# Optimization experiments

Hardware: AMD Instinct MI355X
Metric: run time of the kernel (lower is better)

Reference implementation:

```python
import jax, jax.numpy as jnp
import numpy as np

N_NODES = 50000
N_EDGES = 800000
IN_FEAT = 256
HEADS = 8
D_K = 64


def setup_inputs() -> dict:
    key = jax.random.key(0)
    ks = jax.random.split(key, 6)
    x = jax.random.normal(ks[0], (N_NODES, IN_FEAT), dtype=jnp.float32)
    edge_index = jax.random.randint(ks[1], (2, N_EDGES), 0, N_NODES, dtype=jnp.int32)
    # xavier-uniform linear weights, stored as [in, out] for x @ W
    limit = float(np.sqrt(6.0 / (IN_FEAT + HEADS * D_K)))
    Wq = jax.random.uniform(ks[2], (IN_FEAT, HEADS * D_K), jnp.float32, -limit, limit)
    Wk = jax.random.uniform(ks[3], (IN_FEAT, HEADS * D_K), jnp.float32, -limit, limit)
    Wv = jax.random.uniform(ks[4], (IN_FEAT, HEADS * D_K), jnp.float32, -limit, limit)
    D = jax.random.uniform(ks[5], (HEADS, D_K), jnp.float32, -1.0, 1.0)
    return {"x": x, "edge_index": edge_index, "Wq": Wq, "Wk": Wk, "Wv": Wv, "D": D}


def reference(x, edge_index, Wq, Wk, Wv, D):
    N = x.shape[0]
    H, dk = D.shape
    scale = 1.0 / np.sqrt(dk)

    Q = (x @ Wq).reshape(N, H, dk)
    K = (x @ Wk).reshape(N, H, dk)
    V = (x @ Wv).reshape(N, H, dk)

    row, col = edge_index[0], edge_index[1]
    Ke = K[row]          # [E, H, dk]
    Qe = Q[col]          # [E, H, dk] (for self edges col==row so Q[col]==Q[row])
    diff = Ke - Qe
    s_edge = jnp.einsum('ehd,hd->eh', diff * diff, D)   # diagonal Mahalanobis
    s_self = jnp.einsum('ehd,hd->eh', Ke * Qe, D)       # self-loop score
    scores = jnp.where((row == col)[:, None], s_self, s_edge)
    scores = jax.nn.leaky_relu(scores * scale, negative_slope=0.2)

    # segment softmax over destination node `row` (PyG softmax semantics)
    smax = jax.ops.segment_max(scores, row, num_segments=N)
    smax = jnp.where(jnp.isfinite(smax), smax, 0.0)     # nodes with no incoming edges
    ex = jnp.exp(scores - smax[row])
    denom = jax.ops.segment_sum(ex, row, num_segments=N)
    alpha = ex / (denom[row] + 1e-16)                   # [E, H]

    out = jax.ops.segment_sum(alpha[:, :, None] * V[col], row, num_segments=N)
    return out.reshape(N, H * dk)
```

## Files before the change

kernel.cpp:

```cpp
#include <hip/hip_runtime.h>
#include <hip/hip_bf16.h>

#define N_NODES 50000
#define N_PAD   50176
#define N_EDGES 800000
#define IN_FEAT 256
#define HEADS 8
#define D_K 64
#define HD 512

typedef __hip_bfloat16 bf16;
typedef unsigned int u32;

using bf16x8 = __attribute__((ext_vector_type(8))) short;
using f32x4  = __attribute__((ext_vector_type(4))) float;

#define WS_Q       0
#define WS_K       51200000
#define WS_V       102400000
#define WS_OFFSETS 153600000
#define WS_CURSOR  153800192
#define WS_DEG     154000192
#define WS_CSR     154200192
#define WS_SQ2     157400192
#define WS_AUX     159000192

#define DOUT_XB 0
#define DOUT_WT 25690112

#define SCAN_BLOCKS 49

__device__ __forceinline__ float bflo(u32 u) { return __uint_as_float(u << 16); }
__device__ __forceinline__ float bfhi(u32 u) { return __uint_as_float(u & 0xffff0000u); }

__device__ __forceinline__ void gload16(const void* g, void* l)
{
    __builtin_amdgcn_global_load_lds(
        (const __attribute__((address_space(1))) unsigned int*)g,
        (__attribute__((address_space(3))) unsigned int*)l,
        16, 0, 0);
}

__global__ __launch_bounds__(256) void convert_x(
    const float* __restrict__ x, bf16* __restrict__ xb)
{
    const int t   = blockIdx.x * 256 + threadIdx.x;
    const int row = t >> 5;
    const int c8  = (t & 31) * 8;
    if (row >= N_PAD) return;
    alignas(16) bf16 tmp[8];
    if (row < N_NODES) {
        const float* p = x + (size_t)row * IN_FEAT + c8;
        float4 a = *(const float4*)p;
        float4 b = *(const float4*)(p + 4);
        tmp[0] = __float2bfloat16(a.x); tmp[1] = __float2bfloat16(a.y);
        tmp[2] = __float2bfloat16(a.z); tmp[3] = __float2bfloat16(a.w);
        tmp[4] = __float2bfloat16(b.x); tmp[5] = __float2bfloat16(b.y);
        tmp[6] = __float2bfloat16(b.z); tmp[7] = __float2bfloat16(b.w);
    } else {
#pragma unroll
        for (int i = 0; i < 8; ++i) tmp[i] = __float2bfloat16(0.f);
    }
    *(uint4*)(xb + (size_t)row * IN_FEAT + c8) = *(const uint4*)tmp;
}

__global__ __launch_bounds__(256) void convert_w(
    const float* __restrict__ Wq, const float* __restrict__ Wk, const float* __restrict__ Wv,
    bf16* __restrict__ Wt)
{
    const int t = blockIdx.x * 256 + threadIdx.x;
    if (t >= 3 * 512 * 256) return;
    const int mat = t >> 17;
    const int r   = t & 131071;
    const int n   = r >> 8;
    const int k   = r & 255;
    const float* W = (mat == 0) ? Wq : (mat == 1) ? Wk : Wv;
    Wt[t] = __float2bfloat16(W[k * HD + n]);
}

__global__ __launch_bounds__(256) void mfma_qkv(
    const bf16* __restrict__ xb, const bf16* __restrict__ Wt,
    bf16* __restrict__ Qb, bf16* __restrict__ Kb, bf16* __restrict__ Vb)
{
    __shared__ uint4 Ab4[512];
    __shared__ uint4 Bb4[512];
    char* AbB = (char*)Ab4;
    char* BbB = (char*)Bb4;

    const int tid  = threadIdx.x;
    const int lane = tid & 63;
    const int wid  = tid >> 6;
    const int wr   = wid >> 1;
    const int wc   = wid & 1;

    const int m0  = blockIdx.x * 128;
    const int n0  = blockIdx.y * 128;
    const int mat = blockIdx.z;
    const bf16* __restrict__ wt = Wt + (size_t)mat * 512 * 256;
    bf16* __restrict__ outp = (mat == 0) ? Qb : (mat == 1) ? Kb : Vb;

    const int rch  = lane >> 2;
    const int slot = (lane & 3) ^ (rch & 3);
    const int sc0  = wid;
    const int sc1  = wid + 4;
    const size_t arow0 = (size_t)(m0 + sc0 * 16 + rch) * IN_FEAT + slot * 8;
    const size_t arow1 = (size_t)(m0 + sc1 * 16 + rch) * IN_FEAT + slot * 8;
    const size_t brow0 = (size_t)(n0 + sc0 * 16 + rch) * IN_FEAT + slot * 8;
    const size_t brow1 = (size_t)(n0 + sc1 * 16 + rch) * IN_FEAT + slot * 8;

    const int fr    = lane & 15;
    const int fslot = (((lane >> 4) ^ (lane & 3)) << 4);
    const int abase = (wr * 64 + fr) * 64 + fslot;
    const int bbase = (wc * 64 + fr) * 64 + fslot;

    f32x4 acc[4][4];
#pragma unroll
    for (int i = 0; i < 4; ++i)
#pragma unroll
        for (int j = 0; j < 4; ++j) acc[i][j] = {0.f, 0.f, 0.f, 0.f};

    for (int k0 = 0; k0 < IN_FEAT; k0 += 32) {
        gload16(xb + arow0 + k0, AbB + sc0 * 1024);
        gload16(xb + arow1 + k0, AbB + sc1 * 1024);
        gload16(wt + brow0 + k0, BbB + sc0 * 1024);
        gload16(wt + brow1 + k0, BbB + sc1 * 1024);
        __syncthreads();

        bf16x8 aF[4], bF[4];
#pragma unroll
        for (int m = 0; m < 4; ++m) aF[m] = *(const bf16x8*)(AbB + abase + m * 16 * 64);
#pragma unroll
        for (int n = 0; n < 4; ++n) bF[n] = *(const bf16x8*)(BbB + bbase + n * 16 * 64);
#pragma unroll
        for (int m = 0; m < 4; ++m)
#pragma unroll
            for (int n = 0; n < 4; ++n)
                acc[m][n] = __builtin_amdgcn_mfma_f32_16x16x32_bf16(aF[m], bF[n], acc[m][n], 0, 0, 0);
        __syncthreads();
    }

    const int c_col = lane & 15;
    const int r_hi  = (lane >> 4) * 4;
#pragma unroll
    for (int m = 0; m < 4; ++m) {
        const int grow_base = m0 + wr * 64 + m * 16 + r_hi;
#pragma unroll
        for (int j = 0; j < 4; ++j) {
            const int grow = grow_base + j;
            if (grow < N_NODES) {
#pragma unroll
                for (int n = 0; n < 4; ++n)
                    outp[(size_t)grow * HD + n0 + wc * 64 + n * 16 + c_col] =
                        __float2bfloat16(acc[m][n][j]);
            }
        }
    }
}

__global__ void zero_deg_kernel(int* __restrict__ deg)
{
    int i = blockIdx.x * 256 + threadIdx.x;
    if (i < N_NODES) deg[i] = 0;
}

__global__ void hist_kernel(const int* __restrict__ row, int* __restrict__ deg)
{
    int e = blockIdx.x * 256 + threadIdx.x;
    if (e < N_EDGES) atomicAdd(&deg[row[e]], 1);
}

__global__ __launch_bounds__(1024) void scan_local(const int* __restrict__ deg,
                                                   int* __restrict__ offsets,
                                                   int* __restrict__ aux)
{
    __shared__ int buf[1024];
    const int tid = threadIdx.x;
    const int i = blockIdx.x * 1024 + tid;
    const int v = (i < N_NODES) ? deg[i] : 0;
    buf[tid] = v;
    __syncthreads();
    for (int off = 1; off < 1024; off <<= 1) {
        int t = (tid >= off) ? buf[tid - off] : 0;
        __syncthreads();
        buf[tid] += t;
        __syncthreads();
    }
    if (i < N_NODES) offsets[i] = buf[tid] - v;
    if (tid == 1023) aux[blockIdx.x] = buf[1023];
}

__global__ void scan_aux(int* __restrict__ aux)
{
    const int tid = threadIdx.x;
    const int orig = (tid < SCAN_BLOCKS) ? aux[tid] : 0;
    int v = orig;
    for (int off = 1; off < 64; off <<= 1) {
        int t = __shfl_up(v, off, 64);
        if (tid >= off) v += t;
    }
    if (tid < SCAN_BLOCKS) aux[tid] = v - orig;
}

__global__ __launch_bounds__(1024) void scan_apply(const int* __restrict__ aux,
                                                   int* __restrict__ offsets,
                                                   int* __restrict__ cursor)
{
    const int i = blockIdx.x * 1024 + threadIdx.x;
    if (i < N_NODES) {
        const int off = offsets[i] + aux[i >> 10];
        offsets[i] = off;
        cursor[i]  = off;
    }
    if (i == 0) offsets[N_NODES] = N_EDGES;
}

__global__ void scatter_kernel(const int* __restrict__ row, const int* __restrict__ col,
                               int* __restrict__ cursor, int* __restrict__ csr_col)
{
    int e = blockIdx.x * 256 + threadIdx.x;
    if (e < N_EDGES) {
        const int pos = atomicAdd(&cursor[row[e]], 1);
        csr_col[pos] = col[e];
    }
}

__global__ __launch_bounds__(256) void sq2_kernel(
    const bf16* __restrict__ Qb, const float* __restrict__ Dm, float* __restrict__ sQ2)
{
    const int lane = threadIdx.x & 63;
    const int wid  = threadIdx.x >> 6;
    const int n = blockIdx.x * 4 + wid;
    if (n >= N_NODES) return;

    uint4 qp = *(const uint4*)(Qb + (size_t)n * HD + lane * 8);
    float4 da = *(const float4*)(Dm + lane * 8);
    float4 db = *(const float4*)(Dm + lane * 8 + 4);
    float q0 = bflo(qp.x), q1 = bfhi(qp.x), q2 = bflo(qp.y), q3 = bfhi(qp.y);
    float q4 = bflo(qp.z), q5 = bfhi(qp.z), q6 = bflo(qp.w), q7 = bfhi(qp.w);
    float s = da.x*q0*q0 + da.y*q1*q1 + da.z*q2*q2 + da.w*q3*q3
            + db.x*q4*q4 + db.y*q5*q5 + db.z*q6*q6 + db.w*q7*q7;
    s += __shfl_xor(s, 1, 64);
    s += __shfl_xor(s, 2, 64);
    s += __shfl_xor(s, 4, 64);
    if ((lane & 7) == 0) sQ2[n * 8 + (lane >> 3)] = s;
}

__global__ __launch_bounds__(256) void edge_attn(
    const bf16* __restrict__ Qb, const bf16* __restrict__ Kb, const bf16* __restrict__ Vb,
    const float* __restrict__ Dm, const float* __restrict__ sQ2,
    const int* __restrict__ offsets, const int* __restrict__ csr_col,
    float* __restrict__ out)
{
    __shared__ float dk_lds[4][8][72];

    const int tid  = threadIdx.x;
    const int lane = tid & 63;
    const int wid  = tid >> 6;
    const int r = blockIdx.x * 4 + wid;
    if (r >= N_NODES) return;

    const int hB = lane >> 3;
    const int tB = lane & 7;
    uint4 kp = *(const uint4*)(Kb + (size_t)r * HD + lane * 8);
    float4 da = *(const float4*)(Dm + lane * 8);
    float4 db = *(const float4*)(Dm + lane * 8 + 4);
    float k0 = bflo(kp.x), k1 = bfhi(kp.x), k2 = bflo(kp.y), k3 = bfhi(kp.y);
    float k4 = bflo(kp.z), k5 = bfhi(kp.z), k6 = bflo(kp.w), k7 = bfhi(kp.w);
    float e0_ = da.x*k0, e1_ = da.y*k1, e2_ = da.z*k2, e3_ = da.w*k3;
    float e4_ = db.x*k4, e5_ = db.y*k5, e6_ = db.z*k6, e7_ = db.w*k7;
    float sk = e0_*k0 + e1_*k1 + e2_*k2 + e3_*k3 + e4_*k4 + e5_*k5 + e6_*k6 + e7_*k7;
    sk += __shfl_xor(sk, 1, 64);
    sk += __shfl_xor(sk, 2, 64);
    sk += __shfl_xor(sk, 4, 64);
    float4 w0 = {e0_, e1_, e2_, e3_}, w1 = {e4_, e5_, e6_, e7_};
    *(float4*)&dk_lds[wid][hB][tB * 8]     = w0;
    *(float4*)&dk_lds[wid][hB][tB * 8 + 4] = w1;

    const int hA = lane & 7;
    const int jA = lane >> 3;
    const float sK2_A = __shfl(sk, hA * 8, 64);

    const int s0 = offsets[r];
    const int s1 = offsets[r + 1];

    float m = -INFINITY, l = 0.f;
    float o0=0,o1=0,o2=0,o3=0,o4=0,o5=0,o6=0,o7=0;

    const float* dkrow = &dk_lds[wid][hA][0];

    for (int eb = s0; eb < s1; eb += 8) {
        const int cnt = min(8, s1 - eb);
        const bool act = jA < cnt;
        const int cj = csr_col[eb + min(jA, cnt - 1)];

        const bf16* qrow = Qb + (size_t)cj * HD + hA * D_K;
        float cross = 0.f;
#pragma unroll
        for (int t = 0; t < 8; ++t) {
            uint4 qp = *(const uint4*)(qrow + t * 8);
            float4 ka = *(const float4*)(dkrow + t * 8);
            float4 kb2 = *(const float4*)(dkrow + t * 8 + 4);
            cross += ka.x * bflo(qp.x) + ka.y * bfhi(qp.x)
                   + ka.z * bflo(qp.y) + ka.w * bfhi(qp.y)
                   + kb2.x * bflo(qp.z) + kb2.y * bfhi(qp.z)
                   + kb2.z * bflo(qp.w) + kb2.w * bfhi(qp.w);
        }
        const float sq2 = sQ2[cj * 8 + hA];
        float sraw = (cj == r) ? cross : (sK2_A - 2.f * cross + sq2);
        float s = sraw * 0.125f;
        s = (s < 0.f) ? 0.2f * s : s;
        s = act ? s : -INFINITY;

        float bm = s;
        bm = fmaxf(bm, __shfl_xor(bm, 8, 64));
        bm = fmaxf(bm, __shfl_xor(bm, 16, 64));
        bm = fmaxf(bm, __shfl_xor(bm, 32, 64));
        const float mn   = fmaxf(m, bm);
        const float corr = __expf(m - mn);
        const float w    = __expf(s - mn);
        m = mn;
        float ls = w;
        ls += __shfl_xor(ls, 8, 64);
        ls += __shfl_xor(ls, 16, 64);
        ls += __shfl_xor(ls, 32, 64);
        l = l * corr + ls;

        const float corrB = __shfl(corr, hB, 64);
        o0*=corrB; o1*=corrB; o2*=corrB; o3*=corrB;
        o4*=corrB; o5*=corrB; o6*=corrB; o7*=corrB;
#pragma unroll
        for (int e = 0; e < 8; ++e) {
            const int   ce    = __shfl(cj, e * 8, 64);
            const float alpha = __shfl(w, e * 8 + hB, 64);
            uint4 vp = *(const uint4*)(Vb + (size_t)ce * HD + lane * 8);
            o0 = fmaf(alpha, bflo(vp.x), o0);
            o1 = fmaf(alpha, bfhi(vp.x), o1);
            o2 = fmaf(alpha, bflo(vp.y), o2);
            o3 = fmaf(alpha, bfhi(vp.y), o3);
            o4 = fmaf(alpha, bflo(vp.z), o4);
            o5 = fmaf(alpha, bfhi(vp.z), o5);
            o6 = fmaf(alpha, bflo(vp.w), o6);
            o7 = fmaf(alpha, bfhi(vp.w), o7);
        }
    }

    const float lB  = __shfl(l, hB, 64);
    const float inv = 1.f / (lB + 1e-16f);
    float4 r0 = {o0*inv, o1*inv, o2*inv, o3*inv};
    float4 r1 = {o4*inv, o5*inv, o6*inv, o7*inv};
    *(float4*)(out + (size_t)r * HD + lane * 8)     = r0;
    *(float4*)(out + (size_t)r * HD + lane * 8 + 4) = r1;
}

extern "C" void kernel_launch(void* const* d_in, const int* in_sizes, int n_in,
                              void* d_out, int out_size, void* d_ws, size_t ws_size,
                              hipStream_t stream)
{
    const float* x  = (const float*)d_in[0];
    const int*   ei = (const int*)d_in[1];
    const float* Wq = (const float*)d_in[2];
    const float* Wk = (const float*)d_in[3];
    const float* Wv = (const float*)d_in[4];
    const float* Dm = (const float*)d_in[5];
    float* out = (float*)d_out;

    char* ws = (char*)d_ws;
    bf16* Qb      = (bf16*)(ws + WS_Q);
    bf16* Kb      = (bf16*)(ws + WS_K);
    bf16* Vb      = (bf16*)(ws + WS_V);
    int*  offsets = (int*)(ws + WS_OFFSETS);
    int*  cursor  = (int*)(ws + WS_CURSOR);
    int*  deg     = (int*)(ws + WS_DEG);
    int*  csr_col = (int*)(ws + WS_CSR);
    float* sQ2    = (float*)(ws + WS_SQ2);
    int*  aux     = (int*)(ws + WS_AUX);

    bf16* xb = (bf16*)((char*)d_out + DOUT_XB);
    bf16* Wt = (bf16*)((char*)d_out + DOUT_WT);

    const int* row = ei;
    const int* col = ei + N_EDGES;

    hipLaunchKernelGGL(zero_deg_kernel, dim3((N_NODES + 255) / 256), dim3(256), 0, stream, deg);
    hipLaunchKernelGGL(convert_x, dim3(N_PAD * 32 / 256), dim3(256), 0, stream, x, xb);
    hipLaunchKernelGGL(convert_w, dim3((3 * 512 * 256 + 255) / 256), dim3(256), 0, stream,
                       Wq, Wk, Wv, Wt);
    hipLaunchKernelGGL(hist_kernel, dim3((N_EDGES + 255) / 256), dim3(256), 0, stream, row, deg);
    hipLaunchKernelGGL(mfma_qkv, dim3(N_PAD / 128, 4, 3), dim3(256), 0, stream,
                       xb, Wt, Qb, Kb, Vb);
    hipLaunchKernelGGL(scan_local, dim3(SCAN_BLOCKS), dim3(1024), 0, stream, deg, offsets, aux);
    hipLaunchKernelGGL(scan_aux, dim3(1), dim3(64), 0, stream, aux);
    hipLaunchKernelGGL(scan_apply, dim3(SCAN_BLOCKS), dim3(1024), 0, stream, aux, offsets, cursor);
    hipLaunchKernelGGL(scatter_kernel, dim3((N_EDGES + 255) / 256), dim3(256), 0, stream,
                       row, col, cursor, csr_col);
    hipLaunchKernelGGL(sq2_kernel, dim3((N_NODES + 3) / 4), dim3(256), 0, stream, Qb, Dm, sQ2);
    hipLaunchKernelGGL(edge_attn, dim3((N_NODES + 3) / 4), dim3(256), 0, stream,
                       Qb, Kb, Vb, Dm, sQ2, offsets, csr_col, out);
}
```

Measured before the change: 458.2 us.

## Compute edge scores with coalesced full-row Q loads and persistent waves

The edge-attention kernel now computes each neighbor's score by loading that neighbor's whole Q row with all 64 lanes (one contiguous 1KB read per edge). It then reduces per head with xor shuffles and redistributes the scores with ds_bpermute. Before, each lane gathered a 128-byte head slice across 8 edges, reading K·D from LDS. The LDS staging is removed, partial edge batches skip the inactive loads, and the launch becomes a persistent grid of 1536 blocks that grid-strides over nodes. The trade is more shuffle traffic and serialized per-edge loops in exchange for better-coalesced gathers, plus possible load imbalance from the fixed grid.

```diff
diff --git a/kernel.cpp b/kernel.cpp
--- a/kernel.cpp
+++ b/kernel.cpp
@@ -251,105 +251,106 @@
     const int* __restrict__ offsets, const int* __restrict__ csr_col,
     float* __restrict__ out)
 {
-    __shared__ float dk_lds[4][8][72];
-
-    const int tid  = threadIdx.x;
-    const int lane = tid & 63;
-    const int wid  = tid >> 6;
-    const int r = blockIdx.x * 4 + wid;
-    if (r >= N_NODES) return;
+    const int lane   = threadIdx.x & 63;
+    const int wid    = threadIdx.x >> 6;
+    const int gwave  = blockIdx.x * 4 + wid;
+    const int nwaves = gridDim.x * 4;
 
     const int hB = lane >> 3;
     const int tB = lane & 7;
-    uint4 kp = *(const uint4*)(Kb + (size_t)r * HD + lane * 8);
-    float4 da = *(const float4*)(Dm + lane * 8);
-    float4 db = *(const float4*)(Dm + lane * 8 + 4);
-    float k0 = bflo(kp.x), k1 = bfhi(kp.x), k2 = bflo(kp.y), k3 = bfhi(kp.y);
-    float k4 = bflo(kp.z), k5 = bfhi(kp.z), k6 = bflo(kp.w), k7 = bfhi(kp.w);
-    float e0_ = da.x*k0, e1_ = da.y*k1, e2_ = da.z*k2, e3_ = da.w*k3;
-    float e4_ = db.x*k4, e5_ = db.y*k5, e6_ = db.z*k6, e7_ = db.w*k7;
-    float sk = e0_*k0 + e1_*k1 + e2_*k2 + e3_*k3 + e4_*k4 + e5_*k5 + e6_*k6 + e7_*k7;
-    sk += __shfl_xor(sk, 1, 64);
-    sk += __shfl_xor(sk, 2, 64);
-    sk += __shfl_xor(sk, 4, 64);
-    float4 w0 = {e0_, e1_, e2_, e3_}, w1 = {e4_, e5_, e6_, e7_};
-    *(float4*)&dk_lds[wid][hB][tB * 8]     = w0;
-    *(float4*)&dk_lds[wid][hB][tB * 8 + 4] = w1;
-
-    const int hA = lane & 7;
-    const int jA = lane >> 3;
-    const float sK2_A = __shfl(sk, hA * 8, 64);
-
-    const int s0 = offsets[r];
-    const int s1 = offsets[r + 1];
-
-    float m = -INFINITY, l = 0.f;
-    float o0=0,o1=0,o2=0,o3=0,o4=0,o5=0,o6=0,o7=0;
-
-    const float* dkrow = &dk_lds[wid][hA][0];
-
-    for (int eb = s0; eb < s1; eb += 8) {
-        const int cnt = min(8, s1 - eb);
-        const bool act = jA < cnt;
-        const int cj = csr_col[eb + min(jA, cnt - 1)];
-
-        const bf16* qrow = Qb + (size_t)cj * HD + hA * D_K;
-        float cross = 0.f;
-#pragma unroll
-        for (int t = 0; t < 8; ++t) {
-            uint4 qp = *(const uint4*)(qrow + t * 8);
-            float4 ka = *(const float4*)(dkrow + t * 8);
-            float4 kb2 = *(const float4*)(dkrow + t * 8 + 4);
-            cross += ka.x * bflo(qp.x) + ka.y * bfhi(qp.x)
-                   + ka.z * bflo(qp.y) + ka.w * bfhi(qp.y)
-                   + kb2.x * bflo(qp.z) + kb2.y * bfhi(qp.z)
-                   + kb2.z * bflo(qp.w) + kb2.w * bfhi(qp.w);
+
+    const float4 da = *(const float4*)(Dm + lane * 8);
+    const float4 db = *(const float4*)(Dm + lane * 8 + 4);
+    const int bperm_addr = (((lane & 7) * 8) + (lane >> 3)) << 2;
+
+    for (int r = gwave; r < N_NODES; r += nwaves) {
+        uint4 kp = *(const uint4*)(Kb + (size_t)r * HD + lane * 8);
+        const float k0 = bflo(kp.x), k1 = bfhi(kp.x), k2 = bflo(kp.y), k3 = bfhi(kp.y);
+        const float k4 = bflo(kp.z), k5 = bfhi(kp.z), k6 = bflo(kp.w), k7 = bfhi(kp.w);
+        const float e0 = da.x*k0, e1 = da.y*k1, e2 = da.z*k2, e3 = da.w*k3;
+        const float e4 = db.x*k4, e5 = db.y*k5, e6 = db.z*k6, e7 = db.w*k7;
+        float sk = e0*k0 + e1*k1 + e2*k2 + e3*k3 + e4*k4 + e5*k5 + e6*k6 + e7*k7;
+        sk += __shfl_xor(sk, 1, 64);
+        sk += __shfl_xor(sk, 2, 64);
+        sk += __shfl_xor(sk, 4, 64);
+
+        const int s0o = offsets[r];
+        const int s1o = offsets[r + 1];
+
+        float m = -INFINITY, l = 0.f;
+        float o0=0,o1=0,o2=0,o3=0,o4=0,o5=0,o6=0,o7=0;
+
+        for (int eb = s0o; eb < s1o; eb += 8) {
+            const int cnt = min(8, s1o - eb);
+            const int cv  = csr_col[eb + min(lane, cnt - 1)];
+
+            float val = 0.f;
+#pragma unroll
+            for (int e = 0; e < 8; ++e) {
+                float s;
+                if (e < cnt) {
+                    const int ce = __shfl(cv, e, 64);
+                    uint4 qp = *(const uint4*)(Qb + (size_t)ce * HD + lane * 8);
+                    float cr = e0*bflo(qp.x) + e1*bfhi(qp.x)
+                             + e2*bflo(qp.y) + e3*bfhi(qp.y)
+                             + e4*bflo(qp.z) + e5*bfhi(qp.z)
+                             + e6*bflo(qp.w) + e7*bfhi(qp.w);
+                    cr += __shfl_xor(cr, 1, 64);
+                    cr += __shfl_xor(cr, 2, 64);
+                    cr += __shfl_xor(cr, 4, 64);
+                    const float sq2v = sQ2[ce * 8 + hB];
+                    const float sraw = (ce == r) ? cr : (sk - 2.f * cr + sq2v);
+                    const float y = sraw * 0.125f;
+                    s = fmaxf(y, 0.2f * y);
+                } else {
+                    s = -INFINITY;
+                }
+                if (tB == e) val = s;
+            }
+            const float sA = __int_as_float(
+                __builtin_amdgcn_ds_bpermute(bperm_addr, __float_as_int(val)));
+
+            float bm = sA;
+            bm = fmaxf(bm, __shfl_xor(bm, 8, 64));
+            bm = fmaxf(bm, __shfl_xor(bm, 16, 64));
+            bm = fmaxf(bm, __shfl_xor(bm, 32, 64));
+            const float mn   = fmaxf(m, bm);
+            const float corr = __expf(m - mn);
+            const float w    = __expf(sA - mn);
+            m = mn;
+            float ls = w;
+            ls += __shfl_xor(ls, 8, 64);
+            ls += __shfl_xor(ls, 16, 64);
+            ls += __shfl_xor(ls, 32, 64);
+            l = l * corr + ls;
+
+            const float corrB = __shfl(corr, hB, 64);
+            o0*=corrB; o1*=corrB; o2*=corrB; o3*=corrB;
+            o4*=corrB; o5*=corrB; o6*=corrB; o7*=corrB;
+#pragma unroll
+            for (int e = 0; e < 8; ++e) {
+                if (e >= cnt) break;
+                const int   ce    = __shfl(cv, e, 64);
+                const float alpha = __shfl(w, e * 8 + hB, 64);
+                uint4 vp = *(const uint4*)(Vb + (size_t)ce * HD + lane * 8);
+                o0 = fmaf(alpha, bflo(vp.x), o0);
+                o1 = fmaf(alpha, bfhi(vp.x), o1);
+                o2 = fmaf(alpha, bflo(vp.y), o2);
+                o3 = fmaf(alpha, bfhi(vp.y), o3);
+                o4 = fmaf(alpha, bflo(vp.z), o4);
+                o5 = fmaf(alpha, bfhi(vp.z), o5);
+                o6 = fmaf(alpha, bflo(vp.w), o6);
+                o7 = fmaf(alpha, bfhi(vp.w), o7);
+            }
         }
-        const float sq2 = sQ2[cj * 8 + hA];
-        float sraw = (cj == r) ? cross : (sK2_A - 2.f * cross + sq2);
-        float s = sraw * 0.125f;
-        s = (s < 0.f) ? 0.2f * s : s;
-        s = act ? s : -INFINITY;
-
-        float bm = s;
-        bm = fmaxf(bm, __shfl_xor(bm, 8, 64));
-        bm = fmaxf(bm, __shfl_xor(bm, 16, 64));
-        bm = fmaxf(bm, __shfl_xor(bm, 32, 64));
-        const float mn   = fmaxf(m, bm);
-        const float corr = __expf(m - mn);
-        const float w    = __expf(s - mn);
-        m = mn;
-        float ls = w;
-        ls += __shfl_xor(ls, 8, 64);
-        ls += __shfl_xor(ls, 16, 64);
-        ls += __shfl_xor(ls, 32, 64);
-        l = l * corr + ls;
-
-        const float corrB = __shfl(corr, hB, 64);
-        o0*=corrB; o1*=corrB; o2*=corrB; o3*=corrB;
-        o4*=corrB; o5*=corrB; o6*=corrB; o7*=corrB;
-#pragma unroll
-        for (int e = 0; e < 8; ++e) {
-            const int   ce    = __shfl(cj, e * 8, 64);
-            const float alpha = __shfl(w, e * 8 + hB, 64);
-            uint4 vp = *(const uint4*)(Vb + (size_t)ce * HD + lane * 8);
-            o0 = fmaf(alpha, bflo(vp.x), o0);
-            o1 = fmaf(alpha, bfhi(vp.x), o1);
-            o2 = fmaf(alpha, bflo(vp.y), o2);
-            o3 = fmaf(alpha, bfhi(vp.y), o3);
-            o4 = fmaf(alpha, bflo(vp.z), o4);
-            o5 = fmaf(alpha, bfhi(vp.z), o5);
-            o6 = fmaf(alpha, bflo(vp.w), o6);
-            o7 = fmaf(alpha, bfhi(vp.w), o7);
-        }
-    }
-
-    const float lB  = __shfl(l, hB, 64);
-    const float inv = 1.f / (lB + 1e-16f);
-    float4 r0 = {o0*inv, o1*inv, o2*inv, o3*inv};
-    float4 r1 = {o4*inv, o5*inv, o6*inv, o7*inv};
-    *(float4*)(out + (size_t)r * HD + lane * 8)     = r0;
-    *(float4*)(out + (size_t)r * HD + lane * 8 + 4) = r1;
+
+        const float lB  = __shfl(l, hB, 64);
+        const float inv = 1.f / (lB + 1e-16f);
+        float4 r0 = {o0*inv, o1*inv, o2*inv, o3*inv};
+        float4 r1 = {o4*inv, o5*inv, o6*inv, o7*inv};
+        *(float4*)(out + (size_t)r * HD + lane * 8)     = r0;
+        *(float4*)(out + (size_t)r * HD + lane * 8 + 4) = r1;
+    }
 }
 
 extern "C" void kernel_launch(void* const* d_in, const int* in_sizes, int n_in,
@@ -394,6 +395,6 @@
     hipLaunchKernelGGL(scatter_kernel, dim3((N_EDGES + 255) / 256), dim3(256), 0, stream,
                        row, col, cursor, csr_col);
     hipLaunchKernelGGL(sq2_kernel, dim3((N_NODES + 3) / 4), dim3(256), 0, stream, Qb, Dm, sQ2);
-    hipLaunchKernelGGL(edge_attn, dim3((N_NODES + 3) / 4), dim3(256), 0, stream,
+    hipLaunchKernelGGL(edge_attn, dim3(1536), dim3(256), 0, stream,
                        Qb, Kb, Vb, Dm, sQ2, offsets, csr_col, out);
 }
```

Result: slower. 571.5 us (+24.7%).
